# Performance work log

Hardware: AMD Instinct MI355X
Metric: run time of the kernel (lower is better)

Reference implementation:

```python
import jax, jax.numpy as jnp
import numpy as np

B, L, D, H = 32, 512, 512, 8


def setup_inputs() -> dict:
    key = jax.random.key(0)
    ks = jax.random.split(key, 6)
    s = 0.02
    return {
        "queries": jax.random.normal(ks[0], (B, L, D), jnp.float32),
        "keys": jax.random.normal(ks[1], (B, L, D), jnp.float32),
        "Wq": jax.random.normal(ks[2], (D, D), jnp.float32) * s,
        "bq": jnp.zeros((D,), jnp.float32),
        "Wk": jax.random.normal(ks[3], (D, D), jnp.float32) * s,
        "bk": jnp.zeros((D,), jnp.float32),
        "Wv": jax.random.normal(ks[4], (D, D), jnp.float32) * s,
        "bv": jnp.zeros((D,), jnp.float32),
        "causality": 1,
    }


def reference(queries, keys, Wq, bq, Wk, bk, Wv, bv, causality):
    b, lq, d = queries.shape
    lk = keys.shape[1]
    dh = d // H

    # torch Linear: x @ W.T + b
    Q = queries @ Wq.T + bq
    K = keys @ Wk.T + bk
    V = keys @ Wv.T + bv

    # chunk along feature dim then cat along batch == head-major [H, B, L, dh]
    def split_heads(x, l):
        return x.reshape(b, l, H, dh).transpose(2, 0, 1, 3)

    Qh = split_heads(Q, lq)
    Kh = split_heads(K, lk)
    Vh = split_heads(V, lk)

    scores = jnp.einsum('hbqd,hbkd->hbqk', Qh, Kh) / jnp.sqrt(jnp.asarray(dh, queries.dtype))

    # sign-based key padding mask: zero rows of `keys` get -inf scores
    key_mask = jnp.sign(jnp.sum(jnp.abs(keys), axis=-1))  # [B, Lk]
    scores = jnp.where(key_mask[None, :, None, :] == 0, -jnp.inf, scores)

    if causality:
        tril = jnp.tril(jnp.ones((lq, lk), dtype=bool))
        scores = jnp.where(tril[None, None, :, :], scores, -jnp.inf)

    w = jax.nn.softmax(scores, axis=-1)
    w = jnp.nan_to_num(w, nan=0.0, posinf=0.0, neginf=0.0)

    # sign-based query mask multiplied AFTER softmax
    query_mask = jnp.sign(jnp.sum(jnp.abs(queries), axis=-1))  # [B, Lq]
    w = w * query_mask[None, :, :, None]

    attention_weights = w.transpose(1, 0, 2, 3)  # [B, H, Lq, Lk]

    # dropout is identity in eval mode
    out = jnp.einsum('hbqk,hbkd->hbqd', w, Vh)          # [H, B, Lq, dh]
    out = out.transpose(1, 2, 0, 3).reshape(b, lq, d)    # head-major concat on feature dim
    return out, attention_weights
```

## Files before the change

### kernel.cpp

```cpp
#include <hip/hip_runtime.h>
#include <math.h>

typedef short short8 __attribute__((ext_vector_type(8)));
typedef short short4v __attribute__((ext_vector_type(4)));
typedef float float4v __attribute__((ext_vector_type(4)));

__device__ __forceinline__ short f2bf(float f) {
    union { float f; unsigned u; } v; v.f = f;
    unsigned r = (v.u + 0x7FFFu + ((v.u >> 16) & 1u)) >> 16;
    return (short)r;
}

__device__ __forceinline__ void async16(const short* g, short* l) {
    __builtin_amdgcn_global_load_lds(
        (const __attribute__((address_space(1))) unsigned*)g,
        (__attribute__((address_space(3))) unsigned*)l, 16, 0, 0);
}

__global__ void cvt_kernel(const float* __restrict__ src, short* __restrict__ dst, int n4) {
    int i = blockIdx.x * blockDim.x + threadIdx.x;
    if (i < n4) {
        float4v v = ((const float4v*)src)[i];
        short4v o;
        o[0] = f2bf(v[0]); o[1] = f2bf(v[1]); o[2] = f2bf(v[2]); o[3] = f2bf(v[3]);
        ((short4v*)dst)[i] = o;
    }
}

__global__ __launch_bounds__(256) void cvtmask_kernel(
    const float* __restrict__ q, const float* __restrict__ k,
    short* __restrict__ qb, short* __restrict__ kb,
    float* __restrict__ qm, float* __restrict__ km) {
    int tid = threadIdx.x;
    int lane = tid & 63, wv = tid >> 6;
    int row = blockIdx.x * 4 + wv;
    const float* src; short* dst; float* msk; int r;
    if (row < 16384) { src = q; dst = qb; msk = qm; r = row; }
    else             { src = k; dst = kb; msk = km; r = row - 16384; }
    const float4v* p = (const float4v*)(src + (size_t)r * 512);
    float4v a = p[lane];
    float4v b = p[lane + 64];
    short4v o1, o2;
    o1[0] = f2bf(a[0]); o1[1] = f2bf(a[1]); o1[2] = f2bf(a[2]); o1[3] = f2bf(a[3]);
    o2[0] = f2bf(b[0]); o2[1] = f2bf(b[1]); o2[2] = f2bf(b[2]); o2[3] = f2bf(b[3]);
    short4v* d4 = (short4v*)(dst + (size_t)r * 512);
    d4[lane] = o1;
    d4[lane + 64] = o2;
    float s = fabsf(a[0]) + fabsf(a[1]) + fabsf(a[2]) + fabsf(a[3])
            + fabsf(b[0]) + fabsf(b[1]) + fabsf(b[2]) + fabsf(b[3]);
    #pragma unroll
    for (int off = 1; off < 64; off <<= 1) s += __shfl_xor(s, off, 64);
    if (lane == 0) msk[r] = (s > 0.f) ? 1.f : 0.f;
}

__global__ __launch_bounds__(256) void proj_kernel(
    const short* __restrict__ Xq, const short* __restrict__ Xk,
    const short* __restrict__ Wqp, const short* __restrict__ Wkp, const short* __restrict__ Wvp,
    const float* __restrict__ bqp, const float* __restrict__ bkp, const float* __restrict__ bvp,
    short* __restrict__ Qo, short* __restrict__ Ko, short* __restrict__ Vo) {
    __shared__ short As[128 * 64];
    __shared__ short Bs[128 * 64];
    int z = blockIdx.z;
    const short* X    = (z == 0) ? Xq  : Xk;
    const short* W    = (z == 0) ? Wqp : (z == 1) ? Wkp : Wvp;
    const float* bias = (z == 0) ? bqp : (z == 1) ? bkp : bvp;
    short* out        = (z == 0) ? Qo  : (z == 1) ? Ko  : Vo;

    int tid = threadIdx.x;
    int lane = tid & 63, wv = tid >> 6;
    int col = lane & 15, quad = lane >> 4;
    int m0 = blockIdx.x * 128;
    int n0 = blockIdx.y * 128;
    int msub = (wv & 1) * 64, nsub = (wv >> 1) * 64;

    float4v acc[4][4];
    #pragma unroll
    for (int mt = 0; mt < 4; ++mt)
        #pragma unroll
        for (int nt = 0; nt < 4; ++nt) { acc[mt][nt][0]=0.f; acc[mt][nt][1]=0.f; acc[mt][nt][2]=0.f; acc[mt][nt][3]=0.f; }

    int rowS = tid >> 3;
    int seg  = tid & 7;
    const short* gA = X + (size_t)(m0 + rowS) * 512 + seg * 8;
    const short* gB = W + (size_t)(n0 + rowS) * 512 + seg * 8;
    short* lA = As + (size_t)tid * 8;
    short* lB = Bs + (size_t)tid * 8;

    for (int k0 = 0; k0 < 512; k0 += 64) {
        __syncthreads();
        #pragma unroll
        for (int j = 0; j < 4; ++j) {
            async16(gA + (size_t)(j * 32) * 512 + k0, lA + j * 2048);
            async16(gB + (size_t)(j * 32) * 512 + k0, lB + j * 2048);
        }
        __syncthreads();
        #pragma unroll
        for (int ksub = 0; ksub < 2; ++ksub) {
            short8 a[4], b[4];
            #pragma unroll
            for (int mt = 0; mt < 4; ++mt)
                a[mt] = *(const short8*)(As + (msub + mt * 16 + col) * 64 + ksub * 32 + quad * 8);
            #pragma unroll
            for (int nt = 0; nt < 4; ++nt)
                b[nt] = *(const short8*)(Bs + (nsub + nt * 16 + col) * 64 + ksub * 32 + quad * 8);
            #pragma unroll
            for (int mt = 0; mt < 4; ++mt)
                #pragma unroll
                for (int nt = 0; nt < 4; ++nt)
                    acc[mt][nt] = __builtin_amdgcn_mfma_f32_16x16x32_bf16(a[mt], b[nt], acc[mt][nt], 0, 0, 0);
        }
    }

    #pragma unroll
    for (int nt = 0; nt < 4; ++nt) {
        float bv = bias[n0 + nsub + nt * 16 + col];
        #pragma unroll
        for (int mt = 0; mt < 4; ++mt) {
            #pragma unroll
            for (int r = 0; r < 4; ++r) {
                int m = m0 + msub + mt * 16 + quad * 4 + r;
                out[(size_t)m * 512 + n0 + nsub + nt * 16 + col] = f2bf(acc[mt][nt][r] + bv);
            }
        }
    }
}

__global__ __launch_bounds__(256) void attn_kernel(
    const short* __restrict__ Q, const short* __restrict__ K, const short* __restrict__ V,
    const float* __restrict__ qmask, const float* __restrict__ kmask,
    const int* __restrict__ caus, float* __restrict__ out, float* __restrict__ aw) {
    __shared__ short vt[64 * 520];
    __shared__ short wl[4 * 16 * 72];

    int tid = threadIdx.x;
    int lane = tid & 63, wv = tid >> 6;
    int col = lane & 15, quad = lane >> 4;
    int bh = blockIdx.x, qt = blockIdx.y;
    int b = bh >> 3, h = bh & 7;
    int q0 = qt * 64 + wv * 16;
    size_t rowbase = (size_t)b * 512;
    bool causal = (*caus) != 0;
    int lim = causal ? (qt * 4 + wv) : 31;
    int climit = causal ? qt : 7;

    short8 bQ0, bQ1;
    {
        const short* qp = Q + (rowbase + q0 + col) * 512 + h * 64 + quad * 8;
        bQ0 = *(const short8*)(qp);
        bQ1 = *(const short8*)(qp + 32);
    }

    float4v sc[32];
    const short* kp = K + (rowbase + col) * 512 + h * 64 + quad * 8;
    const float* kmp = kmask + b * 512;
    int qg = q0 + col;
    #pragma unroll
    for (int t = 0; t < 32; ++t) {
        if (t <= lim) {
            short8 aK0 = *(const short8*)(kp + (size_t)(t * 16) * 512);
            short8 aK1 = *(const short8*)(kp + (size_t)(t * 16) * 512 + 32);
            float4v s; s[0]=0.f; s[1]=0.f; s[2]=0.f; s[3]=0.f;
            s = __builtin_amdgcn_mfma_f32_16x16x32_bf16(aK0, bQ0, s, 0, 0, 0);
            s = __builtin_amdgcn_mfma_f32_16x16x32_bf16(aK1, bQ1, s, 0, 0, 0);
            int kb = t * 16 + quad * 4;
            float4v km4 = *(const float4v*)(kmp + kb);
            #pragma unroll
            for (int r = 0; r < 4; ++r) {
                float v = s[r] * 0.125f;
                bool masked = (km4[r] == 0.f) || (causal && (kb + r > qg));
                sc[t][r] = masked ? -INFINITY : v;
            }
        } else {
            sc[t][0]=0.f; sc[t][1]=0.f; sc[t][2]=0.f; sc[t][3]=0.f;
        }
    }

    float mx = -INFINITY;
    #pragma unroll
    for (int t = 0; t < 32; ++t)
        if (t <= lim) {
            #pragma unroll
            for (int r = 0; r < 4; ++r) mx = fmaxf(mx, sc[t][r]);
        }
    mx = fmaxf(mx, __shfl_xor(mx, 16, 64));
    mx = fmaxf(mx, __shfl_xor(mx, 32, 64));
    float sm = 0.f;
    #pragma unroll
    for (int t = 0; t < 32; ++t)
        if (t <= lim) {
            #pragma unroll
            for (int r = 0; r < 4; ++r) {
                float s = sc[t][r];
                float e = (s == -INFINITY) ? 0.f : __expf(s - mx);
                sc[t][r] = e;
                sm += e;
            }
        }
    sm += __shfl_xor(sm, 16, 64);
    sm += __shfl_xor(sm, 32, 64);
    float qmv = qmask[b * 512 + qg];
    float inv = (sm > 0.f) ? (qmv / sm) : 0.f;

    {
        float* awr = aw + ((size_t)b * 8 + h) * 512 * 512 + (size_t)qg * 512 + quad * 4;
        float4v z4; z4[0]=0.f; z4[1]=0.f; z4[2]=0.f; z4[3]=0.f;
        #pragma unroll
        for (int t = 0; t < 32; ++t) {
            if (t <= lim) {
                #pragma unroll
                for (int r = 0; r < 4; ++r) sc[t][r] *= inv;
                __builtin_nontemporal_store(sc[t], (float4v*)(awr + t * 16));
            } else {
                __builtin_nontemporal_store(z4, (float4v*)(awr + t * 16));
            }
        }
    }

    #pragma unroll
    for (int c = 0; c < 8; ++c) {
        if (c <= climit) {
            #pragma unroll
            for (int i = 0; i < 2; ++i) {
                int idx = i * 256 + tid;
                int kk = idx >> 3, sg = idx & 7;
                short8 v8 = *(const short8*)(V + (rowbase + c * 64 + kk) * 512 + h * 64 + sg * 8);
                int ck = (c * 64 + kk) ^ (sg << 3);
                #pragma unroll
                for (int j = 0; j < 8; ++j)
                    vt[(sg * 8 + j) * 520 + ck] = v8[j];
            }
        }
    }
    __syncthreads();

    float4v O[4];
    #pragma unroll
    for (int nt = 0; nt < 4; ++nt) { O[nt][0]=0.f; O[nt][1]=0.f; O[nt][2]=0.f; O[nt][3]=0.f; }
    short* wlw = wl + wv * (16 * 72);
    #pragma unroll
    for (int c = 0; c < 8; ++c) {
        if (c <= climit) {
            #pragma unroll
            for (int tl = 0; tl < 4; ++tl) {
                int t = c * 4 + tl;
                short4v w4;
                #pragma unroll
                for (int r = 0; r < 4; ++r) w4[r] = f2bf(sc[t][r]);
                *(short4v*)(wlw + col * 72 + tl * 16 + quad * 4) = w4;
            }
            #pragma unroll
            for (int sub = 0; sub < 2; ++sub) {
                short8 aW = *(const short8*)(wlw + col * 72 + sub * 32 + quad * 8);
                #pragma unroll
                for (int nt = 0; nt < 4; ++nt) {
                    int d = nt * 16 + col;
                    int cb = (c * 64 + sub * 32 + quad * 8) ^ (((d >> 3) & 7) << 3);
                    short8 bV = *(const short8*)(vt + d * 520 + cb);
                    O[nt] = __builtin_amdgcn_mfma_f32_16x16x32_bf16(aW, bV, O[nt], 0, 0, 0);
                }
            }
        }
    }
    #pragma unroll
    for (int nt = 0; nt < 4; ++nt) {
        #pragma unroll
        for (int r = 0; r < 4; ++r) {
            int qq = q0 + quad * 4 + r;
            __builtin_nontemporal_store(O[nt][r],
                out + (rowbase + qq) * 512 + h * 64 + nt * 16 + col);
        }
    }
}

extern "C" void kernel_launch(void* const* d_in, const int* in_sizes, int n_in,
                              void* d_out, int out_size, void* d_ws, size_t ws_size,
                              hipStream_t stream) {
    const float* queries = (const float*)d_in[0];
    const float* keys    = (const float*)d_in[1];
    const float* Wq      = (const float*)d_in[2];
    const float* bq      = (const float*)d_in[3];
    const float* Wk      = (const float*)d_in[4];
    const float* bk      = (const float*)d_in[5];
    const float* Wv      = (const float*)d_in[6];
    const float* bv      = (const float*)d_in[7];
    const int*   caus    = (const int*)d_in[8];

    const size_t NE = (size_t)16384 * 512;
    short* qbf = (short*)d_ws;
    short* kbf = qbf + NE;
    short* Qb  = kbf + NE;
    short* Kb  = Qb + NE;
    short* Vb  = Kb + NE;
    short* wqb = Vb + NE;
    short* wkb = wqb + 512 * 512;
    short* wvb = wkb + 512 * 512;
    float* qm  = (float*)(wvb + 512 * 512);
    float* km  = qm + 32 * 512;

    cvtmask_kernel<<<8192, 256, 0, stream>>>(queries, keys, qbf, kbf, qm, km);
    cvt_kernel<<<256, 256, 0, stream>>>(Wq, wqb, 65536);
    cvt_kernel<<<256, 256, 0, stream>>>(Wk, wkb, 65536);
    cvt_kernel<<<256, 256, 0, stream>>>(Wv, wvb, 65536);
    dim3 pg(128, 4, 3);
    proj_kernel<<<pg, 256, 0, stream>>>(qbf, kbf, wqb, wkb, wvb, bq, bk, bv, Qb, Kb, Vb);
    float* outp = (float*)d_out;
    float* awp  = outp + 8388608;
    dim3 ag(256, 8);
    attn_kernel<<<ag, 256, 0, stream>>>(Qb, Kb, Vb, qm, km, caus, outp, awp);
}
```

Before: 516.0 us.

## Use two-pass online softmax with QK recompute and double-buffered V tiles

```diff
diff --git a/kernel.cpp b/kernel.cpp
--- a/kernel.cpp
+++ b/kernel.cpp
@@ -17,14 +17,18 @@
         (__attribute__((address_space(3))) unsigned*)l, 16, 0, 0);
 }
 
-__global__ void cvt_kernel(const float* __restrict__ src, short* __restrict__ dst, int n4) {
+__global__ __launch_bounds__(256) void cvt3_kernel(
+    const float* __restrict__ w0, const float* __restrict__ w1, const float* __restrict__ w2,
+    short* __restrict__ d0, short* __restrict__ d1, short* __restrict__ d2) {
     int i = blockIdx.x * blockDim.x + threadIdx.x;
-    if (i < n4) {
-        float4v v = ((const float4v*)src)[i];
-        short4v o;
-        o[0] = f2bf(v[0]); o[1] = f2bf(v[1]); o[2] = f2bf(v[2]); o[3] = f2bf(v[3]);
-        ((short4v*)dst)[i] = o;
-    }
+    int sel = i >> 16;
+    int j = i & 65535;
+    const float* src = (sel == 0) ? w0 : (sel == 1) ? w1 : w2;
+    short* dst       = (sel == 0) ? d0 : (sel == 1) ? d1 : d2;
+    float4v v = ((const float4v*)src)[j];
+    short4v o;
+    o[0] = f2bf(v[0]); o[1] = f2bf(v[1]); o[2] = f2bf(v[2]); o[3] = f2bf(v[3]);
+    ((short4v*)dst)[j] = o;
 }
 
 __global__ __launch_bounds__(256) void cvtmask_kernel(
@@ -129,7 +133,7 @@
     const short* __restrict__ Q, const short* __restrict__ K, const short* __restrict__ V,
     const float* __restrict__ qmask, const float* __restrict__ kmask,
     const int* __restrict__ caus, float* __restrict__ out, float* __restrict__ aw) {
-    __shared__ short vt[64 * 520];
+    __shared__ short vtb[2][64 * 72];
     __shared__ short wl[4 * 16 * 72];
 
     int tid = threadIdx.x;
@@ -150,10 +154,12 @@
         bQ1 = *(const short8*)(qp + 32);
     }
 
-    float4v sc[32];
     const short* kp = K + (rowbase + col) * 512 + h * 64 + quad * 8;
     const float* kmp = kmask + b * 512;
     int qg = q0 + col;
+    const float C = 0.125f * 1.44269504089f;
+
+    float m = -INFINITY, l = 0.f;
     #pragma unroll
     for (int t = 0; t < 32; ++t) {
         if (t <= lim) {
@@ -164,88 +170,88 @@
             s = __builtin_amdgcn_mfma_f32_16x16x32_bf16(aK1, bQ1, s, 0, 0, 0);
             int kb = t * 16 + quad * 4;
             float4v km4 = *(const float4v*)(kmp + kb);
-            #pragma unroll
-            for (int r = 0; r < 4; ++r) {
-                float v = s[r] * 0.125f;
-                bool masked = (km4[r] == 0.f) || (causal && (kb + r > qg));
-                sc[t][r] = masked ? -INFINITY : v;
-            }
-        } else {
-            sc[t][0]=0.f; sc[t][1]=0.f; sc[t][2]=0.f; sc[t][3]=0.f;
-        }
-    }
-
-    float mx = -INFINITY;
-    #pragma unroll
-    for (int t = 0; t < 32; ++t)
-        if (t <= lim) {
-            #pragma unroll
-            for (int r = 0; r < 4; ++r) mx = fmaxf(mx, sc[t][r]);
-        }
-    mx = fmaxf(mx, __shfl_xor(mx, 16, 64));
-    mx = fmaxf(mx, __shfl_xor(mx, 32, 64));
-    float sm = 0.f;
-    #pragma unroll
-    for (int t = 0; t < 32; ++t)
-        if (t <= lim) {
-            #pragma unroll
-            for (int r = 0; r < 4; ++r) {
-                float s = sc[t][r];
-                float e = (s == -INFINITY) ? 0.f : __expf(s - mx);
-                sc[t][r] = e;
-                sm += e;
-            }
-        }
-    sm += __shfl_xor(sm, 16, 64);
-    sm += __shfl_xor(sm, 32, 64);
+            float e0, e1, e2, e3, tmax;
+            e0 = ((km4[0] != 0.f) && (!causal || (kb + 0 <= qg))) ? s[0] * C : -INFINITY;
+            e1 = ((km4[1] != 0.f) && (!causal || (kb + 1 <= qg))) ? s[1] * C : -INFINITY;
+            e2 = ((km4[2] != 0.f) && (!causal || (kb + 2 <= qg))) ? s[2] * C : -INFINITY;
+            e3 = ((km4[3] != 0.f) && (!causal || (kb + 3 <= qg))) ? s[3] * C : -INFINITY;
+            tmax = fmaxf(fmaxf(e0, e1), fmaxf(e2, e3));
+            float nm = fmaxf(m, tmax);
+            float f = (m == -INFINITY) ? 0.f : exp2f(m - nm);
+            float ls = 0.f;
+            ls += (e0 == -INFINITY) ? 0.f : exp2f(e0 - nm);
+            ls += (e1 == -INFINITY) ? 0.f : exp2f(e1 - nm);
+            ls += (e2 == -INFINITY) ? 0.f : exp2f(e2 - nm);
+            ls += (e3 == -INFINITY) ? 0.f : exp2f(e3 - nm);
+            l = l * f + ls;
+            m = nm;
+        }
+    }
+    #pragma unroll
+    for (int off = 16; off <= 32; off <<= 1) {
+        float mo = __shfl_xor(m, off, 64);
+        float lo = __shfl_xor(l, off, 64);
+        float M = fmaxf(m, mo);
+        float fa = (m  == -INFINITY) ? 0.f : exp2f(m - M);
+        float fb = (mo == -INFINITY) ? 0.f : exp2f(mo - M);
+        l = l * fa + lo * fb;
+        m = M;
+    }
     float qmv = qmask[b * 512 + qg];
-    float inv = (sm > 0.f) ? (qmv / sm) : 0.f;
-
-    {
-        float* awr = aw + ((size_t)b * 8 + h) * 512 * 512 + (size_t)qg * 512 + quad * 4;
-        float4v z4; z4[0]=0.f; z4[1]=0.f; z4[2]=0.f; z4[3]=0.f;
-        #pragma unroll
-        for (int t = 0; t < 32; ++t) {
-            if (t <= lim) {
-                #pragma unroll
-                for (int r = 0; r < 4; ++r) sc[t][r] *= inv;
-                __builtin_nontemporal_store(sc[t], (float4v*)(awr + t * 16));
-            } else {
-                __builtin_nontemporal_store(z4, (float4v*)(awr + t * 16));
-            }
-        }
-    }
+    float inv = (l > 0.f) ? (qmv / l) : 0.f;
+
+    int kk0 = tid >> 3, sgv = tid & 7;
+    const short* vp = V + rowbase * 512 + h * 64 + sgv * 8;
+    int lck0 = kk0 ^ (sgv << 3);
+    int lck1 = (kk0 + 32) ^ (sgv << 3);
+    short8 pva = *(const short8*)(vp + (size_t)(kk0) * 512);
+    short8 pvb = *(const short8*)(vp + (size_t)(kk0 + 32) * 512);
+
+    float4v O[4];
+    #pragma unroll
+    for (int nt = 0; nt < 4; ++nt) { O[nt][0]=0.f; O[nt][1]=0.f; O[nt][2]=0.f; O[nt][3]=0.f; }
+    short* wlw = wl + wv * (16 * 72);
+    float* awr = aw + ((size_t)b * 8 + h) * 512 * 512 + (size_t)qg * 512 + quad * 4;
+    float4v z4; z4[0]=0.f; z4[1]=0.f; z4[2]=0.f; z4[3]=0.f;
 
     #pragma unroll
     for (int c = 0; c < 8; ++c) {
         if (c <= climit) {
-            #pragma unroll
-            for (int i = 0; i < 2; ++i) {
-                int idx = i * 256 + tid;
-                int kk = idx >> 3, sg = idx & 7;
-                short8 v8 = *(const short8*)(V + (rowbase + c * 64 + kk) * 512 + h * 64 + sg * 8);
-                int ck = (c * 64 + kk) ^ (sg << 3);
-                #pragma unroll
-                for (int j = 0; j < 8; ++j)
-                    vt[(sg * 8 + j) * 520 + ck] = v8[j];
+            short* vb = &vtb[c & 1][0];
+            #pragma unroll
+            for (int j = 0; j < 8; ++j) vb[(sgv * 8 + j) * 72 + lck0] = pva[j];
+            #pragma unroll
+            for (int j = 0; j < 8; ++j) vb[(sgv * 8 + j) * 72 + lck1] = pvb[j];
+            __syncthreads();
+            if (c + 1 <= climit) {
+                pva = *(const short8*)(vp + (size_t)((c + 1) * 64 + kk0) * 512);
+                pvb = *(const short8*)(vp + (size_t)((c + 1) * 64 + kk0 + 32) * 512);
             }
-        }
-    }
-    __syncthreads();
-
-    float4v O[4];
-    #pragma unroll
-    for (int nt = 0; nt < 4; ++nt) { O[nt][0]=0.f; O[nt][1]=0.f; O[nt][2]=0.f; O[nt][3]=0.f; }
-    short* wlw = wl + wv * (16 * 72);
-    #pragma unroll
-    for (int c = 0; c < 8; ++c) {
-        if (c <= climit) {
             #pragma unroll
             for (int tl = 0; tl < 4; ++tl) {
                 int t = c * 4 + tl;
                 short4v w4;
-                #pragma unroll
-                for (int r = 0; r < 4; ++r) w4[r] = f2bf(sc[t][r]);
+                if (t <= lim) {
+                    short8 aK0 = *(const short8*)(kp + (size_t)(t * 16) * 512);
+                    short8 aK1 = *(const short8*)(kp + (size_t)(t * 16) * 512 + 32);
+                    float4v s; s[0]=0.f; s[1]=0.f; s[2]=0.f; s[3]=0.f;
+                    s = __builtin_amdgcn_mfma_f32_16x16x32_bf16(aK0, bQ0, s, 0, 0, 0);
+                    s = __builtin_amdgcn_mfma_f32_16x16x32_bf16(aK1, bQ1, s, 0, 0, 0);
+                    int kb = t * 16 + quad * 4;
+                    float4v km4 = *(const float4v*)(kmp + kb);
+                    float4v w;
+                    #pragma unroll
+                    for (int r = 0; r < 4; ++r) {
+                        bool ok = (km4[r] != 0.f) && (!causal || (kb + r <= qg)) && (inv > 0.f);
+                        float wvv = ok ? exp2f(s[r] * C - m) * inv : 0.f;
+                        w[r] = wvv;
+                        w4[r] = f2bf(wvv);
+                    }
+                    __builtin_nontemporal_store(w, (float4v*)(awr + t * 16));
+                } else {
+                    w4[0]=0; w4[1]=0; w4[2]=0; w4[3]=0;
+                    __builtin_nontemporal_store(z4, (float4v*)(awr + t * 16));
+                }
                 *(short4v*)(wlw + col * 72 + tl * 16 + quad * 4) = w4;
             }
             #pragma unroll
@@ -254,13 +260,18 @@
                 #pragma unroll
                 for (int nt = 0; nt < 4; ++nt) {
                     int d = nt * 16 + col;
-                    int cb = (c * 64 + sub * 32 + quad * 8) ^ (((d >> 3) & 7) << 3);
-                    short8 bV = *(const short8*)(vt + d * 520 + cb);
+                    int cb = (sub * 32 + quad * 8) ^ (((d >> 3) & 7) << 3);
+                    short8 bV = *(const short8*)(vb + d * 72 + cb);
                     O[nt] = __builtin_amdgcn_mfma_f32_16x16x32_bf16(aW, bV, O[nt], 0, 0, 0);
                 }
             }
-        }
-    }
+        } else {
+            #pragma unroll
+            for (int tl = 0; tl < 4; ++tl)
+                __builtin_nontemporal_store(z4, (float4v*)(awr + (c * 4 + tl) * 16));
+        }
+    }
+
     #pragma unroll
     for (int nt = 0; nt < 4; ++nt) {
         #pragma unroll
@@ -298,9 +309,7 @@
     float* km  = qm + 32 * 512;
 
     cvtmask_kernel<<<8192, 256, 0, stream>>>(queries, keys, qbf, kbf, qm, km);
-    cvt_kernel<<<256, 256, 0, stream>>>(Wq, wqb, 65536);
-    cvt_kernel<<<256, 256, 0, stream>>>(Wk, wkb, 65536);
-    cvt_kernel<<<256, 256, 0, stream>>>(Wv, wvb, 65536);
+    cvt3_kernel<<<768, 256, 0, stream>>>(Wq, Wk, Wv, wqb, wkb, wvb);
     dim3 pg(128, 4, 3);
     proj_kernel<<<pg, 256, 0, stream>>>(qbf, kbf, wqb, wkb, wvb, bq, bk, bv, Qb, Kb, Vb);
     float* outp = (float*)d_out;
```

After: 500.9 us. 1.03x faster.
